# Kernel optimization log

Measured on AMD Instinct MI355X. Metric: run time of the kernel, lower is better.

## Reference

```python
import jax, jax.numpy as jnp
import numpy as np

B, T, E, A, D, S, N, K = 256, 64, 1024, 32, 1024, 256, 1024, 5
MIN_STD = 0.1


def setup_inputs() -> dict:
    key = jax.random.key(0)
    ks = jax.random.split(key, 16)
    def w(k, shape, scale=0.02):
        return jax.random.normal(k, shape, jnp.float32) * scale
    return dict(
        seq_len=T,
        obs_embed=jax.random.normal(ks[0], (B, T, E), jnp.float32),
        action=jax.random.normal(ks[1], (B, T, A), jnp.float32),
        nonterms=jnp.ones((B, T, 1), jnp.float32),
        init_deter=jax.random.normal(ks[2], (B, D), jnp.float32),
        init_stoch=jax.random.normal(ks[3], (B, S), jnp.float32),
        noise_prior=jax.random.normal(ks[4], (T - 1, B, S), jnp.float32),
        noise_post=jax.random.normal(ks[5], (T - 1, B, S), jnp.float32),
        W_embed=w(ks[6], (S + A, D)), b_embed=jnp.zeros((D,), jnp.float32),
        W_ens=w(ks[7], (K, D, S)), b_ens=jnp.zeros((K, S), jnp.float32),
        W_ih=w(ks[8], (3 * D, D)), W_hh=w(ks[9], (3 * D, D)),
        b_ih=jnp.zeros((3 * D,), jnp.float32), b_hh=jnp.zeros((3 * D,), jnp.float32),
        Wp1=w(ks[10], (D, N)), bp1=jnp.zeros((N,), jnp.float32),
        Wp2=w(ks[11], (N, 2 * S)), bp2=jnp.zeros((2 * S,), jnp.float32),
        Wq1=w(ks[12], (D + E, N)), bq1=jnp.zeros((N,), jnp.float32),
        Wq2=w(ks[13], (N, 2 * S)), bq2=jnp.zeros((2 * S,), jnp.float32),
    )


def _rollout(obs_embed, action, nonterms, init_deter, init_stoch,
             noise_prior, noise_post, W_embed, b_embed, W_ens, b_ens,
             W_ih, W_hh, b_ih, b_hh, Wp1, bp1, Wp2, bp2, Wq1, bq1, Wq2, bq2):
    elu = jax.nn.elu

    def gru(x, h):  # torch.nn.GRUCell math
        gi = x @ W_ih.T + b_ih
        gh = h @ W_hh.T + b_hh
        ir, iz, ig = jnp.split(gi, 3, axis=-1)
        hr, hz, hg = jnp.split(gh, 3, axis=-1)
        r = jax.nn.sigmoid(ir + hr)
        z = jax.nn.sigmoid(iz + hz)
        n = jnp.tanh(ig + r * hg)
        return (1.0 - z) * n + z * h

    def step(carry, xs):
        deter, stoch = carry
        obs_t, act_t, nt, eps_p, eps_q = xs  # nt: [B,1]
        prev_action = act_t * nt
        sa = elu(jnp.concatenate([stoch * nt, prev_action], -1) @ W_embed + b_embed)
        preds = jnp.einsum('bd,kds->kbs', sa, W_ens) + b_ens[:, None, :]  # ensemble heads
        deter_new = gru(sa, deter * nt)
        pm, ps = jnp.split(elu(deter_new @ Wp1 + bp1) @ Wp2 + bp2, 2, -1)
        ps = jax.nn.softplus(ps) + MIN_STD
        prior_stoch = pm + ps * eps_p
        qm, qs = jnp.split(elu(jnp.concatenate([deter_new, obs_t], -1) @ Wq1 + bq1) @ Wq2 + bq2, 2, -1)
        qs = jax.nn.softplus(qs) + MIN_STD
        post_stoch = qm + qs * eps_q
        prior_cat = jnp.concatenate([pm, ps, prior_stoch, deter_new], -1)   # [B, 3S+D]
        post_cat = jnp.concatenate([qm, qs, post_stoch, deter_new], -1)     # [B, 3S+D]
        disag_flat = jnp.transpose(preds, (1, 0, 2)).reshape(preds.shape[1], -1)  # [B, K*S]
        out = jnp.concatenate([prior_cat, post_cat, disag_flat], -1)
        return (deter_new, post_stoch), out

    Tm1 = noise_prior.shape[0]
    xs = (jnp.swapaxes(obs_embed[:, :Tm1], 0, 1),
          jnp.swapaxes(action[:, :Tm1], 0, 1),
          jnp.swapaxes(nonterms[:, :Tm1], 0, 1),
          noise_prior, noise_post)
    _, outs = jax.lax.scan(step, (init_deter, init_stoch), xs)
    return jnp.swapaxes(outs, 0, 1)  # [B, T-1, 2*(3S+D)+K*S]


def reference(seq_len, obs_embed, action, nonterms, init_deter, init_stoch,
              noise_prior, noise_post, W_embed, b_embed, W_ens, b_ens,
              W_ih, W_hh, b_ih, b_hh, Wp1, bp1, Wp2, bp2, Wq1, bq1, Wq2, bq2):
    return _rollout(obs_embed, action, nonterms, init_deter, init_stoch,
                    noise_prior, noise_post, W_embed, b_embed, W_ens, b_ens,
                    W_ih, W_hh, b_ih, b_hh, Wp1, bp1, Wp2, bp2, Wq1, bq1, Wq2, bq2)
```

## Files before the change

kernel.cpp:

```cpp
#include <hip/hip_runtime.h>

typedef float f32x4 __attribute__((ext_vector_type(4)));
typedef __bf16 bf16x8 __attribute__((ext_vector_type(8)));
typedef unsigned short u16;

#define NB 256
#define TT 64
#define TM1 63
#define DD 1024
#define SS 256
#define EE 1024
#define AD 32
#define OUTC 4864
#define OUTT ((size_t)TM1 * OUTC)

__device__ __forceinline__ u16 f2bf(float f) {
    unsigned u = __float_as_uint(f);
    u += 0x7FFFu + ((u >> 16) & 1u);
    return (u16)(u >> 16);
}
__device__ __forceinline__ float sigm(float x) { return 1.f / (1.f + expf(-x)); }
__device__ __forceinline__ float splus(float x) { return x > 15.f ? x : log1pf(expf(x)); }
__device__ __forceinline__ float eluf(float x) { return x > 0.f ? x : (expf(x) - 1.f); }
__device__ __forceinline__ int swz(int row, int cb) { return row * 128 + (cb ^ ((row & 7) << 4)); }

template <class FA, class FE>
__device__ __forceinline__ void gemm_tile(char* As, char* Bs, FA fa,
                                          const u16* __restrict__ Bt, int ldb,
                                          int K, int m0, int n0, FE fe) {
    const int tid = threadIdx.x;
    const int lane = tid & 63;
    const int w = tid >> 6;
    const int wr = (w >> 1) * 32, wc = (w & 1) * 32;
    f32x4 acc00 = {}, acc01 = {}, acc10 = {}, acc11 = {};
    const int r0 = tid >> 3;
    const int ke = (tid & 7) * 8;
    const int cb = (tid & 7) * 16;

    for (int k0 = 0; k0 < K; k0 += 64) {
        uint4 av0 = fa(m0 + r0, k0 + ke);
        uint4 av1 = fa(m0 + r0 + 32, k0 + ke);
        uint4 bv0 = *(const uint4*)(Bt + (size_t)(n0 + r0) * ldb + k0 + ke);
        uint4 bv1 = *(const uint4*)(Bt + (size_t)(n0 + r0 + 32) * ldb + k0 + ke);
        __syncthreads();
        *(uint4*)(As + swz(r0, cb)) = av0;
        *(uint4*)(As + swz(r0 + 32, cb)) = av1;
        *(uint4*)(Bs + swz(r0, cb)) = bv0;
        *(uint4*)(Bs + swz(r0 + 32, cb)) = bv1;
        __syncthreads();
#pragma unroll
        for (int kk = 0; kk < 64; kk += 32) {
            const int fcb = kk * 2 + (lane >> 4) * 16;
            bf16x8 a0 = *(const bf16x8*)(As + swz(wr + (lane & 15), fcb));
            bf16x8 a1 = *(const bf16x8*)(As + swz(wr + 16 + (lane & 15), fcb));
            bf16x8 b0 = *(const bf16x8*)(Bs + swz(wc + (lane & 15), fcb));
            bf16x8 b1 = *(const bf16x8*)(Bs + swz(wc + 16 + (lane & 15), fcb));
            acc00 = __builtin_amdgcn_mfma_f32_16x16x32_bf16(a0, b0, acc00, 0, 0, 0);
            acc01 = __builtin_amdgcn_mfma_f32_16x16x32_bf16(a0, b1, acc01, 0, 0, 0);
            acc10 = __builtin_amdgcn_mfma_f32_16x16x32_bf16(a1, b0, acc10, 0, 0, 0);
            acc11 = __builtin_amdgcn_mfma_f32_16x16x32_bf16(a1, b1, acc11, 0, 0, 0);
        }
    }
    const int er = (lane >> 4) * 4, ec = lane & 15;
#pragma unroll
    for (int r = 0; r < 4; r++) {
        fe(m0 + wr + er + r, n0 + wc + ec, acc00[r]);
        fe(m0 + wr + er + r, n0 + wc + 16 + ec, acc01[r]);
        fe(m0 + wr + 16 + er + r, n0 + wc + ec, acc10[r]);
        fe(m0 + wr + 16 + er + r, n0 + wc + 16 + ec, acc11[r]);
    }
}

__global__ void __launch_bounds__(256) k_cast(const float* __restrict__ in,
                                              u16* __restrict__ out, int n) {
    int i = blockIdx.x * 256 + threadIdx.x;
    if (i < n) out[i] = f2bf(in[i]);
}

__global__ void __launch_bounds__(256) k_transpose(const float* __restrict__ in,
                                                   u16* __restrict__ out,
                                                   int R, int C, int Rpad, int total) {
    int i = blockIdx.x * 256 + threadIdx.x;
    if (i >= total) return;
    int r = i % Rpad;
    int bc = i / Rpad;
    int c = bc % C;
    int bb = bc / C;
    out[i] = (r < R) ? f2bf(in[((size_t)bb * R + r) * C + c]) : (u16)0;
}

__global__ void __launch_bounds__(256) k_prep0(const float* __restrict__ init_deter,
                                               const float* __restrict__ init_stoch,
                                               const float* __restrict__ action,
                                               const float* __restrict__ nonterms,
                                               float* __restrict__ deter,
                                               u16* __restrict__ h_nt,
                                               u16* __restrict__ x_embed) {
    int idx = blockIdx.x * 256 + threadIdx.x;
    int b = idx >> 10, d = idx & 1023;
    float nt0 = nonterms[b * TT + 0];
    float dv = init_deter[idx];
    deter[idx] = dv;
    h_nt[idx] = f2bf(dv * nt0);
    if (d < 256) {
        x_embed[b * 320 + d] = f2bf(init_stoch[b * 256 + d] * nt0);
    } else if (d < 320) {
        int c = d - 256;
        x_embed[b * 320 + d] = (c < AD) ? f2bf(action[(size_t)b * TT * AD + c] * nt0) : (u16)0;
    }
}

__global__ void __launch_bounds__(256) k_gru(const float* __restrict__ gi,
                                             const float* __restrict__ gh,
                                             float* __restrict__ deter,
                                             const float* __restrict__ nonterms, int t,
                                             u16* __restrict__ deter_b,
                                             float* __restrict__ out) {
    int idx = blockIdx.x * 256 + threadIdx.x;
    int b = idx >> 10, d = idx & 1023;
    float nt = nonterms[b * TT + t];
    float h = deter[idx] * nt;
    size_t gb = (size_t)b * 3072;
    float r = sigm(gi[gb + d] + gh[gb + d]);
    float z = sigm(gi[gb + 1024 + d] + gh[gb + 1024 + d]);
    float n = tanhf(gi[gb + 2048 + d] + r * gh[gb + 2048 + d]);
    float dn = (1.f - z) * n + z * h;
    deter[idx] = dn;
    deter_b[idx] = f2bf(dn);
    float* ob = out + (size_t)b * OUTT + (size_t)t * OUTC;
    ob[768 + d] = dn;
    ob[2560 + d] = dn;
}

__global__ void __launch_bounds__(256) k_dist(const float* __restrict__ pout,
                                              const float* __restrict__ qout,
                                              const float* __restrict__ noise_p,
                                              const float* __restrict__ noise_q, int t,
                                              const float* __restrict__ deter,
                                              const float* __restrict__ action,
                                              const float* __restrict__ nonterms,
                                              float* __restrict__ out,
                                              u16* __restrict__ x_embed,
                                              u16* __restrict__ h_nt) {
    int idx = blockIdx.x * 256 + threadIdx.x;
    int b = idx >> 10, d = idx & 1023;
    float ntn = nonterms[b * TT + (t + 1)];
    h_nt[idx] = f2bf(deter[idx] * ntn);
    float* ob = out + (size_t)b * OUTT + (size_t)t * OUTC;
    if (d < 256) {
        int s = d;
        float pm = pout[b * 512 + s];
        float ps = splus(pout[b * 512 + 256 + s]) + 0.1f;
        float ep = noise_p[(size_t)t * (NB * SS) + b * SS + s];
        float pst = pm + ps * ep;
        ob[s] = pm;
        ob[256 + s] = ps;
        ob[512 + s] = pst;
        float qm = qout[b * 512 + s];
        float qs = splus(qout[b * 512 + 256 + s]) + 0.1f;
        float eq = noise_q[(size_t)t * (NB * SS) + b * SS + s];
        float qst = qm + qs * eq;
        ob[1792 + s] = qm;
        ob[2048 + s] = qs;
        ob[2304 + s] = qst;
        x_embed[b * 320 + s] = f2bf(qst * ntn);
    } else if (d < 320) {
        int c = d - 256;
        u16 v = 0;
        if (c < AD) v = f2bf(action[(size_t)b * TT * AD + (size_t)(t + 1) * AD + c] * ntn);
        x_embed[b * 320 + 256 + c] = v;
    }
}

__global__ void __launch_bounds__(256) k_gemm_sa(const u16* __restrict__ xe,
                                                 const u16* __restrict__ Wt,
                                                 const float* __restrict__ bias,
                                                 u16* __restrict__ sa) {
    __shared__ char As[8192];
    __shared__ char Bs[8192];
    int m0 = blockIdx.y * 64, n0 = blockIdx.x * 64;
    auto fa = [&](int r, int k) { return *(const uint4*)(xe + r * 320 + k); };
    auto fe = [&](int r, int n, float v) {
        v = eluf(v + bias[n]);
        sa[r * 1024 + n] = f2bf(v);
    };
    gemm_tile(As, Bs, fa, Wt, 320, 320, m0, n0, fe);
}

__global__ void __launch_bounds__(256) k_gemm_big(const u16* __restrict__ sa,
                                                  const u16* __restrict__ hnt,
                                                  const u16* __restrict__ Wih,
                                                  const u16* __restrict__ Whh,
                                                  const u16* __restrict__ Wens,
                                                  const float* __restrict__ bih,
                                                  const float* __restrict__ bhh,
                                                  const float* __restrict__ bens,
                                                  float* __restrict__ gi,
                                                  float* __restrict__ gh,
                                                  float* __restrict__ dout, int t) {
    __shared__ char As[8192];
    __shared__ char Bs[8192];
    int z = blockIdx.z;
    int m0 = blockIdx.y * 64, n0 = blockIdx.x * 64;
    if (z == 2 && n0 >= 1280) return;
    const u16* Ap = (z == 1) ? hnt : sa;
    auto fa = [&](int r, int k) { return *(const uint4*)(Ap + r * 1024 + k); };
    if (z == 0) {
        auto fe = [&](int r, int n, float v) { gi[(size_t)r * 3072 + n] = v + bih[n]; };
        gemm_tile(As, Bs, fa, Wih, 1024, 1024, m0, n0, fe);
    } else if (z == 1) {
        auto fe = [&](int r, int n, float v) { gh[(size_t)r * 3072 + n] = v + bhh[n]; };
        gemm_tile(As, Bs, fa, Whh, 1024, 1024, m0, n0, fe);
    } else {
        float* op = dout + (size_t)t * OUTC + 3584;
        auto fe = [&](int r, int n, float v) { op[(size_t)r * OUTT + n] = v + bens[n]; };
        gemm_tile(As, Bs, fa, Wens, 1024, 1024, m0, n0, fe);
    }
}

__global__ void __launch_bounds__(256) k_gemm_hpq(const u16* __restrict__ dtb,
                                                  const float* __restrict__ obs,
                                                  const u16* __restrict__ Wp1t,
                                                  const u16* __restrict__ Wq1t,
                                                  const float* __restrict__ bp1,
                                                  const float* __restrict__ bq1,
                                                  u16* __restrict__ hp,
                                                  u16* __restrict__ hq, int t) {
    __shared__ char As[8192];
    __shared__ char Bs[8192];
    int z = blockIdx.z;
    int m0 = blockIdx.y * 64, n0 = blockIdx.x * 64;
    if (z == 0) {
        auto fa = [&](int r, int k) { return *(const uint4*)(dtb + r * 1024 + k); };
        auto fe = [&](int r, int n, float v) {
            v = eluf(v + bp1[n]);
            hp[r * 1024 + n] = f2bf(v);
        };
        gemm_tile(As, Bs, fa, Wp1t, 1024, 1024, m0, n0, fe);
    } else {
        auto fa = [&](int r, int k) {
            if (k < 1024) return *(const uint4*)(dtb + r * 1024 + k);
            const float* q = obs + (size_t)r * (TT * EE) + (size_t)t * EE + (k - 1024);
            float4 f0 = *(const float4*)q, f1 = *(const float4*)(q + 4);
            union { u16 u[8]; uint4 v; } x;
            x.u[0] = f2bf(f0.x); x.u[1] = f2bf(f0.y); x.u[2] = f2bf(f0.z); x.u[3] = f2bf(f0.w);
            x.u[4] = f2bf(f1.x); x.u[5] = f2bf(f1.y); x.u[6] = f2bf(f1.z); x.u[7] = f2bf(f1.w);
            return x.v;
        };
        auto fe = [&](int r, int n, float v) {
            v = eluf(v + bq1[n]);
            hq[r * 1024 + n] = f2bf(v);
        };
        gemm_tile(As, Bs, fa, Wq1t, 2048, 2048, m0, n0, fe);
    }
}

__global__ void __launch_bounds__(256) k_gemm_pq(const u16* __restrict__ hp,
                                                 const u16* __restrict__ hq,
                                                 const u16* __restrict__ Wp2t,
                                                 const u16* __restrict__ Wq2t,
                                                 const float* __restrict__ bp2,
                                                 const float* __restrict__ bq2,
                                                 float* __restrict__ pout,
                                                 float* __restrict__ qout) {
    __shared__ char As[8192];
    __shared__ char Bs[8192];
    int z = blockIdx.z;
    int m0 = blockIdx.y * 64, n0 = blockIdx.x * 64;
    const u16* Ap = z ? hq : hp;
    const u16* Bp = z ? Wq2t : Wp2t;
    const float* bb = z ? bq2 : bp2;
    float* op = z ? qout : pout;
    auto fa = [&](int r, int k) { return *(const uint4*)(Ap + r * 1024 + k); };
    auto fe = [&](int r, int n, float v) { op[r * 512 + n] = v + bb[n]; };
    gemm_tile(As, Bs, fa, Bp, 1024, 1024, m0, n0, fe);
}

extern "C" void kernel_launch(void* const* d_in, const int* in_sizes, int n_in,
                              void* d_out, int out_size, void* d_ws, size_t ws_size,
                              hipStream_t stream) {
    const float* obs = (const float*)d_in[1];
    const float* action = (const float*)d_in[2];
    const float* nonterms = (const float*)d_in[3];
    const float* init_deter = (const float*)d_in[4];
    const float* init_stoch = (const float*)d_in[5];
    const float* noise_p = (const float*)d_in[6];
    const float* noise_q = (const float*)d_in[7];
    const float* W_embed = (const float*)d_in[8];
    const float* b_embed = (const float*)d_in[9];
    const float* W_ens = (const float*)d_in[10];
    const float* b_ens = (const float*)d_in[11];
    const float* W_ih = (const float*)d_in[12];
    const float* W_hh = (const float*)d_in[13];
    const float* b_ih = (const float*)d_in[14];
    const float* b_hh = (const float*)d_in[15];
    const float* Wp1 = (const float*)d_in[16];
    const float* bp1 = (const float*)d_in[17];
    const float* Wp2 = (const float*)d_in[18];
    const float* bp2 = (const float*)d_in[19];
    const float* Wq1 = (const float*)d_in[20];
    const float* bq1 = (const float*)d_in[21];
    const float* Wq2 = (const float*)d_in[22];
    const float* bq2 = (const float*)d_in[23];
    float* out = (float*)d_out;

    char* ws = (char*)d_ws;
    size_t off = 0;
    auto alloc = [&](size_t bytes) {
        void* p = ws + off;
        off += (bytes + 255) & ~(size_t)255;
        return p;
    };
    u16* Wembed_t = (u16*)alloc(1024 * 320 * 2);
    u16* Wih_b = (u16*)alloc(3072 * 1024 * 2);
    u16* Whh_b = (u16*)alloc(3072 * 1024 * 2);
    u16* Wens_t = (u16*)alloc(1280 * 1024 * 2);
    u16* Wp1_t = (u16*)alloc(1024 * 1024 * 2);
    u16* Wp2_t = (u16*)alloc(512 * 1024 * 2);
    u16* Wq1_t = (u16*)alloc((size_t)1024 * 2048 * 2);
    u16* Wq2_t = (u16*)alloc(512 * 1024 * 2);
    u16* x_embed = (u16*)alloc(256 * 320 * 2);
    u16* h_nt = (u16*)alloc(256 * 1024 * 2);
    u16* sa = (u16*)alloc(256 * 1024 * 2);
    float* deter = (float*)alloc(256 * 1024 * 4);
    u16* deter_b = (u16*)alloc(256 * 1024 * 2);
    float* gi = (float*)alloc((size_t)256 * 3072 * 4);
    float* gh = (float*)alloc((size_t)256 * 3072 * 4);
    u16* hp = (u16*)alloc(256 * 1024 * 2);
    u16* hq = (u16*)alloc(256 * 1024 * 2);
    float* pout = (float*)alloc(256 * 512 * 4);
    float* qout = (float*)alloc(256 * 512 * 4);
    (void)ws_size;

    {
        int tot = 1024 * 320;
        k_transpose<<<(tot + 255) / 256, 256, 0, stream>>>(W_embed, Wembed_t, 288, 1024, 320, tot);
        int nc = 3072 * 1024;
        k_cast<<<(nc + 255) / 256, 256, 0, stream>>>(W_ih, Wih_b, nc);
        k_cast<<<(nc + 255) / 256, 256, 0, stream>>>(W_hh, Whh_b, nc);
        tot = 5 * 256 * 1024;
        k_transpose<<<(tot + 255) / 256, 256, 0, stream>>>(W_ens, Wens_t, 1024, 256, 1024, tot);
        tot = 1024 * 1024;
        k_transpose<<<(tot + 255) / 256, 256, 0, stream>>>(Wp1, Wp1_t, 1024, 1024, 1024, tot);
        tot = 512 * 1024;
        k_transpose<<<(tot + 255) / 256, 256, 0, stream>>>(Wp2, Wp2_t, 1024, 512, 1024, tot);
        tot = 1024 * 2048;
        k_transpose<<<(tot + 255) / 256, 256, 0, stream>>>(Wq1, Wq1_t, 2048, 1024, 2048, tot);
        tot = 512 * 1024;
        k_transpose<<<(tot + 255) / 256, 256, 0, stream>>>(Wq2, Wq2_t, 1024, 512, 1024, tot);
    }

    k_prep0<<<1024, 256, 0, stream>>>(init_deter, init_stoch, action, nonterms,
                                      deter, h_nt, x_embed);

    for (int t = 0; t < TM1; t++) {
        k_gemm_sa<<<dim3(16, 4), 256, 0, stream>>>(x_embed, Wembed_t, b_embed, sa);
        k_gemm_big<<<dim3(48, 4, 3), 256, 0, stream>>>(sa, h_nt, Wih_b, Whh_b, Wens_t,
                                                       b_ih, b_hh, b_ens, gi, gh, out, t);
        k_gru<<<1024, 256, 0, stream>>>(gi, gh, deter, nonterms, t, deter_b, out);
        k_gemm_hpq<<<dim3(16, 4, 2), 256, 0, stream>>>(deter_b, obs, Wp1_t, Wq1_t,
                                                       bp1, bq1, hp, hq, t);
        k_gemm_pq<<<dim3(8, 4, 2), 256, 0, stream>>>(hp, hq, Wp2_t, Wq2_t, bp2, bq2,
                                                     pout, qout);
        k_dist<<<1024, 256, 0, stream>>>(pout, qout, noise_p, noise_q, t, deter,
                                         action, nonterms, out, x_embed, h_nt);
    }
}
```

Baseline: 4.888 ms.

## Hoist non-recurrent GEMMs out of the time loop and batch them across steps

Restructures the rollout so only the recurrent path stays inside the per-step loop. The observation part of the posterior MLP is computed for all steps up front, and the ensemble heads and prior MLP are run in large batched GEMMs after the loop from stored sa and deter histories. The change also register-prefetches the next K-slice in the GEMM tile, computes several N tiles per block, fuses the softplus/sampling into GEMM epilogues, and switches to fast exp/log/tanh. This removes kernel launches and small-GEMM underutilization per step, at the cost of large history buffers and slightly lower transcendental accuracy.

```diff
diff --git a/kernel.cpp b/kernel.cpp
--- a/kernel.cpp
+++ b/kernel.cpp
@@ -4,70 +4,97 @@
 typedef __bf16 bf16x8 __attribute__((ext_vector_type(8)));
 typedef unsigned short u16;
 
-#define NB 256
-#define TT 64
-#define TM1 63
-#define DD 1024
-#define SS 256
-#define EE 1024
-#define AD 32
 #define OUTC 4864
-#define OUTT ((size_t)TM1 * OUTC)
+#define OUTT ((size_t)63 * OUTC)
 
 __device__ __forceinline__ u16 f2bf(float f) {
     unsigned u = __float_as_uint(f);
     u += 0x7FFFu + ((u >> 16) & 1u);
     return (u16)(u >> 16);
 }
-__device__ __forceinline__ float sigm(float x) { return 1.f / (1.f + expf(-x)); }
-__device__ __forceinline__ float splus(float x) { return x > 15.f ? x : log1pf(expf(x)); }
-__device__ __forceinline__ float eluf(float x) { return x > 0.f ? x : (expf(x) - 1.f); }
+__device__ __forceinline__ float bf2f(u16 h) { return __uint_as_float((unsigned)h << 16); }
+__device__ __forceinline__ float fexp(float x) { return __expf(x); }
+__device__ __forceinline__ float eluf(float x) { return x > 0.f ? x : fexp(x) - 1.f; }
+__device__ __forceinline__ float splus(float x) { return x > 15.f ? x : __logf(1.f + fexp(x)); }
+__device__ __forceinline__ float sigm(float x) { return 1.f / (1.f + fexp(-x)); }
+__device__ __forceinline__ float tanhfast(float x) { return 2.f / (1.f + fexp(-2.f * x)) - 1.f; }
 __device__ __forceinline__ int swz(int row, int cb) { return row * 128 + (cb ^ ((row & 7) << 4)); }
 
-template <class FA, class FE>
-__device__ __forceinline__ void gemm_tile(char* As, char* Bs, FA fa,
-                                          const u16* __restrict__ Bt, int ldb,
-                                          int K, int m0, int n0, FE fe) {
+template <int NT, class FA, class FE>
+__device__ __forceinline__ void gemmN(char* As, FA fa, const u16* __restrict__ Bt,
+                                      int ldb, int n0, int nstr, int K, int m0, FE fe) {
+    char* Bs = As + 8192;
     const int tid = threadIdx.x;
     const int lane = tid & 63;
     const int w = tid >> 6;
     const int wr = (w >> 1) * 32, wc = (w & 1) * 32;
-    f32x4 acc00 = {}, acc01 = {}, acc10 = {}, acc11 = {};
+    f32x4 acc[NT][4];
+    f32x4 zf = {0.f, 0.f, 0.f, 0.f};
+#pragma unroll
+    for (int j = 0; j < NT; j++)
+#pragma unroll
+        for (int q = 0; q < 4; q++) acc[j][q] = zf;
     const int r0 = tid >> 3;
     const int ke = (tid & 7) * 8;
     const int cb = (tid & 7) * 16;
-
+    uint4 av0 = fa(m0 + r0, ke);
+    uint4 av1 = fa(m0 + r0 + 32, ke);
+    uint4 bv[NT][2];
+#pragma unroll
+    for (int j = 0; j < NT; j++) {
+        bv[j][0] = *(const uint4*)(Bt + (size_t)(n0 + j * nstr + r0) * ldb + ke);
+        bv[j][1] = *(const uint4*)(Bt + (size_t)(n0 + j * nstr + r0 + 32) * ldb + ke);
+    }
     for (int k0 = 0; k0 < K; k0 += 64) {
-        uint4 av0 = fa(m0 + r0, k0 + ke);
-        uint4 av1 = fa(m0 + r0 + 32, k0 + ke);
-        uint4 bv0 = *(const uint4*)(Bt + (size_t)(n0 + r0) * ldb + k0 + ke);
-        uint4 bv1 = *(const uint4*)(Bt + (size_t)(n0 + r0 + 32) * ldb + k0 + ke);
         __syncthreads();
         *(uint4*)(As + swz(r0, cb)) = av0;
         *(uint4*)(As + swz(r0 + 32, cb)) = av1;
-        *(uint4*)(Bs + swz(r0, cb)) = bv0;
-        *(uint4*)(Bs + swz(r0 + 32, cb)) = bv1;
+#pragma unroll
+        for (int j = 0; j < NT; j++) {
+            char* B = Bs + j * 8192;
+            *(uint4*)(B + swz(r0, cb)) = bv[j][0];
+            *(uint4*)(B + swz(r0 + 32, cb)) = bv[j][1];
+        }
         __syncthreads();
+        if (k0 + 64 < K) {
+            int k1 = k0 + 64 + ke;
+            av0 = fa(m0 + r0, k1);
+            av1 = fa(m0 + r0 + 32, k1);
+#pragma unroll
+            for (int j = 0; j < NT; j++) {
+                bv[j][0] = *(const uint4*)(Bt + (size_t)(n0 + j * nstr + r0) * ldb + k1);
+                bv[j][1] = *(const uint4*)(Bt + (size_t)(n0 + j * nstr + r0 + 32) * ldb + k1);
+            }
+        }
 #pragma unroll
         for (int kk = 0; kk < 64; kk += 32) {
             const int fcb = kk * 2 + (lane >> 4) * 16;
             bf16x8 a0 = *(const bf16x8*)(As + swz(wr + (lane & 15), fcb));
             bf16x8 a1 = *(const bf16x8*)(As + swz(wr + 16 + (lane & 15), fcb));
-            bf16x8 b0 = *(const bf16x8*)(Bs + swz(wc + (lane & 15), fcb));
-            bf16x8 b1 = *(const bf16x8*)(Bs + swz(wc + 16 + (lane & 15), fcb));
-            acc00 = __builtin_amdgcn_mfma_f32_16x16x32_bf16(a0, b0, acc00, 0, 0, 0);
-            acc01 = __builtin_amdgcn_mfma_f32_16x16x32_bf16(a0, b1, acc01, 0, 0, 0);
-            acc10 = __builtin_amdgcn_mfma_f32_16x16x32_bf16(a1, b0, acc10, 0, 0, 0);
-            acc11 = __builtin_amdgcn_mfma_f32_16x16x32_bf16(a1, b1, acc11, 0, 0, 0);
+#pragma unroll
+            for (int j = 0; j < NT; j++) {
+                char* B = Bs + j * 8192;
+                bf16x8 b0 = *(const bf16x8*)(B + swz(wc + (lane & 15), fcb));
+                bf16x8 b1 = *(const bf16x8*)(B + swz(wc + 16 + (lane & 15), fcb));
+                acc[j][0] = __builtin_amdgcn_mfma_f32_16x16x32_bf16(a0, b0, acc[j][0], 0, 0, 0);
+                acc[j][1] = __builtin_amdgcn_mfma_f32_16x16x32_bf16(a0, b1, acc[j][1], 0, 0, 0);
+                acc[j][2] = __builtin_amdgcn_mfma_f32_16x16x32_bf16(a1, b0, acc[j][2], 0, 0, 0);
+                acc[j][3] = __builtin_amdgcn_mfma_f32_16x16x32_bf16(a1, b1, acc[j][3], 0, 0, 0);
+            }
         }
     }
     const int er = (lane >> 4) * 4, ec = lane & 15;
 #pragma unroll
-    for (int r = 0; r < 4; r++) {
-        fe(m0 + wr + er + r, n0 + wc + ec, acc00[r]);
-        fe(m0 + wr + er + r, n0 + wc + 16 + ec, acc01[r]);
-        fe(m0 + wr + 16 + er + r, n0 + wc + ec, acc10[r]);
-        fe(m0 + wr + 16 + er + r, n0 + wc + 16 + ec, acc11[r]);
+    for (int q = 0; q < 4; q++) {
+        int rr = m0 + wr + (q >> 1) * 16 + er;
+        int cc = n0 + wc + (q & 1) * 16 + ec;
+#pragma unroll
+        for (int r = 0; r < 4; r++) {
+            float vals[NT];
+#pragma unroll
+            for (int j = 0; j < NT; j++) vals[j] = acc[j][q][r];
+            fe(rr + r, cc, vals);
+        }
     }
 }
 
@@ -89,16 +116,16 @@
     out[i] = (r < R) ? f2bf(in[((size_t)bb * R + r) * C + c]) : (u16)0;
 }
 
-__global__ void __launch_bounds__(256) k_prep0(const float* __restrict__ init_deter,
-                                               const float* __restrict__ init_stoch,
-                                               const float* __restrict__ action,
-                                               const float* __restrict__ nonterms,
-                                               float* __restrict__ deter,
-                                               u16* __restrict__ h_nt,
-                                               u16* __restrict__ x_embed) {
+__global__ void __launch_bounds__(256) k_init(const float* __restrict__ init_deter,
+                                              const float* __restrict__ init_stoch,
+                                              const float* __restrict__ action,
+                                              const float* __restrict__ nonterms,
+                                              float* __restrict__ deter,
+                                              u16* __restrict__ h_nt,
+                                              u16* __restrict__ x_embed) {
     int idx = blockIdx.x * 256 + threadIdx.x;
     int b = idx >> 10, d = idx & 1023;
-    float nt0 = nonterms[b * TT + 0];
+    float nt0 = nonterms[b * 64];
     float dv = init_deter[idx];
     deter[idx] = dv;
     h_nt[idx] = f2bf(dv * nt0);
@@ -106,174 +133,205 @@
         x_embed[b * 320 + d] = f2bf(init_stoch[b * 256 + d] * nt0);
     } else if (d < 320) {
         int c = d - 256;
-        x_embed[b * 320 + d] = (c < AD) ? f2bf(action[(size_t)b * TT * AD + c] * nt0) : (u16)0;
-    }
+        x_embed[b * 320 + d] = (c < 32) ? f2bf(action[(size_t)b * 2048 + c] * nt0) : (u16)0;
+    }
+}
+
+__global__ void __launch_bounds__(256) k_obsc(const float* __restrict__ obs,
+                                              const u16* __restrict__ Wq1o_t,
+                                              u16* __restrict__ OBSC) {
+    __shared__ char sm[40960];
+    int jid = blockIdx.x;
+    int rb = jid >> 2, cg = jid & 3;
+    int m0 = rb * 64, n0 = cg * 256;
+    auto fa = [&](int r, int k) {
+        int tt = r >> 8, bb = r & 255;
+        const float* p = obs + ((size_t)bb * 64 + tt) * 1024 + k;
+        float4 f0 = *(const float4*)p, f1 = *(const float4*)(p + 4);
+        union { u16 h[8]; uint4 q; } x;
+        x.h[0] = f2bf(f0.x); x.h[1] = f2bf(f0.y); x.h[2] = f2bf(f0.z); x.h[3] = f2bf(f0.w);
+        x.h[4] = f2bf(f1.x); x.h[5] = f2bf(f1.y); x.h[6] = f2bf(f1.z); x.h[7] = f2bf(f1.w);
+        return x.q;
+    };
+    auto fe = [&](int r, int n, const float* v) {
+#pragma unroll
+        for (int j = 0; j < 4; j++) OBSC[(size_t)r * 1024 + n + j * 64] = f2bf(v[j]);
+    };
+    gemmN<4>(sm, fa, Wq1o_t, 1024, n0, 64, 1024, m0, fe);
+}
+
+__global__ void __launch_bounds__(256) k_sa(const u16* __restrict__ xe,
+                                            const u16* __restrict__ Wt,
+                                            const float* __restrict__ bias,
+                                            u16* __restrict__ sa) {
+    __shared__ char sm[16384];
+    int m0 = blockIdx.y * 64, n0 = blockIdx.x * 64;
+    auto fa = [&](int r, int k) { return *(const uint4*)(xe + r * 320 + k); };
+    auto fe = [&](int r, int n, const float* v) {
+        sa[r * 1024 + n] = f2bf(eluf(v[0] + bias[n]));
+    };
+    gemmN<1>(sm, fa, Wt, 320, n0, 0, 320, m0, fe);
+}
+
+__global__ void __launch_bounds__(256) k_gemm3072(const u16* __restrict__ A,
+                                                  const u16* __restrict__ B,
+                                                  const float* __restrict__ bias,
+                                                  float* __restrict__ dst) {
+    __shared__ char sm[16384];
+    int m0 = blockIdx.y * 64, n0 = blockIdx.x * 64;
+    auto fa = [&](int r, int k) { return *(const uint4*)(A + r * 1024 + k); };
+    auto fe = [&](int r, int n, const float* v) { dst[(size_t)r * 3072 + n] = v[0] + bias[n]; };
+    gemmN<1>(sm, fa, B, 1024, n0, 0, 1024, m0, fe);
 }
 
 __global__ void __launch_bounds__(256) k_gru(const float* __restrict__ gi,
                                              const float* __restrict__ gh,
                                              float* __restrict__ deter,
                                              const float* __restrict__ nonterms, int t,
-                                             u16* __restrict__ deter_b,
+                                             u16* __restrict__ deter_hist,
+                                             u16* __restrict__ h_nt,
                                              float* __restrict__ out) {
     int idx = blockIdx.x * 256 + threadIdx.x;
     int b = idx >> 10, d = idx & 1023;
-    float nt = nonterms[b * TT + t];
+    float nt = nonterms[b * 64 + t];
     float h = deter[idx] * nt;
     size_t gb = (size_t)b * 3072;
     float r = sigm(gi[gb + d] + gh[gb + d]);
     float z = sigm(gi[gb + 1024 + d] + gh[gb + 1024 + d]);
-    float n = tanhf(gi[gb + 2048 + d] + r * gh[gb + 2048 + d]);
+    float n = tanhfast(gi[gb + 2048 + d] + r * gh[gb + 2048 + d]);
     float dn = (1.f - z) * n + z * h;
     deter[idx] = dn;
-    deter_b[idx] = f2bf(dn);
+    u16 db = f2bf(dn);
+    deter_hist[(size_t)t * 262144 + idx] = db;
+    h_nt[idx] = f2bf(dn * nonterms[b * 64 + t + 1]);
     float* ob = out + (size_t)b * OUTT + (size_t)t * OUTC;
     ob[768 + d] = dn;
     ob[2560 + d] = dn;
 }
 
-__global__ void __launch_bounds__(256) k_dist(const float* __restrict__ pout,
-                                              const float* __restrict__ qout,
-                                              const float* __restrict__ noise_p,
-                                              const float* __restrict__ noise_q, int t,
-                                              const float* __restrict__ deter,
-                                              const float* __restrict__ action,
-                                              const float* __restrict__ nonterms,
-                                              float* __restrict__ out,
-                                              u16* __restrict__ x_embed,
-                                              u16* __restrict__ h_nt) {
-    int idx = blockIdx.x * 256 + threadIdx.x;
-    int b = idx >> 10, d = idx & 1023;
-    float ntn = nonterms[b * TT + (t + 1)];
-    h_nt[idx] = f2bf(deter[idx] * ntn);
-    float* ob = out + (size_t)b * OUTT + (size_t)t * OUTC;
-    if (d < 256) {
-        int s = d;
-        float pm = pout[b * 512 + s];
-        float ps = splus(pout[b * 512 + 256 + s]) + 0.1f;
-        float ep = noise_p[(size_t)t * (NB * SS) + b * SS + s];
-        float pst = pm + ps * ep;
-        ob[s] = pm;
-        ob[256 + s] = ps;
-        ob[512 + s] = pst;
-        float qm = qout[b * 512 + s];
-        float qs = splus(qout[b * 512 + 256 + s]) + 0.1f;
-        float eq = noise_q[(size_t)t * (NB * SS) + b * SS + s];
-        float qst = qm + qs * eq;
-        ob[1792 + s] = qm;
-        ob[2048 + s] = qs;
-        ob[2304 + s] = qst;
-        x_embed[b * 320 + s] = f2bf(qst * ntn);
-    } else if (d < 320) {
-        int c = d - 256;
-        u16 v = 0;
-        if (c < AD) v = f2bf(action[(size_t)b * TT * AD + (size_t)(t + 1) * AD + c] * ntn);
-        x_embed[b * 320 + 256 + c] = v;
-    }
-}
-
-__global__ void __launch_bounds__(256) k_gemm_sa(const u16* __restrict__ xe,
-                                                 const u16* __restrict__ Wt,
-                                                 const float* __restrict__ bias,
-                                                 u16* __restrict__ sa) {
-    __shared__ char As[8192];
-    __shared__ char Bs[8192];
+__global__ void __launch_bounds__(256) k_step4(const u16* __restrict__ h_nt,
+                                               const u16* __restrict__ Whh_b,
+                                               const float* __restrict__ b_hh,
+                                               float* __restrict__ gh,
+                                               const u16* __restrict__ deter_hist,
+                                               const u16* __restrict__ Wq1d_t,
+                                               const float* __restrict__ bq1,
+                                               const u16* __restrict__ OBSC,
+                                               u16* __restrict__ HQ, int t) {
+    __shared__ char sm[16384];
+    int bid = blockIdx.x;
+    if (bid < 192) {
+        if (t >= 62) return;
+        int m0 = (bid / 48) * 64, n0 = (bid % 48) * 64;
+        auto fa = [&](int r, int k) { return *(const uint4*)(h_nt + r * 1024 + k); };
+        auto fe = [&](int r, int n, const float* v) { gh[(size_t)r * 3072 + n] = v[0] + b_hh[n]; };
+        gemmN<1>(sm, fa, Whh_b, 1024, n0, 0, 1024, m0, fe);
+    } else {
+        int j = bid - 192;
+        int m0 = (j / 16) * 64, n0 = (j % 16) * 64;
+        const u16* A = deter_hist + (size_t)t * 262144;
+        const u16* ob = OBSC + (size_t)t * 262144;
+        auto fa = [&](int r, int k) { return *(const uint4*)(A + r * 1024 + k); };
+        auto fe = [&](int r, int n, const float* v) {
+            HQ[r * 1024 + n] = f2bf(eluf(v[0] + bq1[n] + bf2f(ob[r * 1024 + n])));
+        };
+        gemmN<1>(sm, fa, Wq1d_t, 1024, n0, 0, 1024, m0, fe);
+    }
+}
+
+__global__ void __launch_bounds__(256) k_q2dist(const u16* __restrict__ HQ,
+                                                const u16* __restrict__ Wq2_t,
+                                                const float* __restrict__ bq2,
+                                                const float* __restrict__ noise_q,
+                                                const float* __restrict__ nonterms,
+                                                const float* __restrict__ action,
+                                                float* __restrict__ out,
+                                                u16* __restrict__ x_embed, int t) {
+    __shared__ char sm[24576];
+    int bid = blockIdx.x;
+    if (bid < 16) {
+        int m0 = (bid >> 2) * 64, n0 = (bid & 3) * 64;
+        auto fa = [&](int r, int k) { return *(const uint4*)(HQ + r * 1024 + k); };
+        auto fe = [&](int r, int s, const float* v) {
+            float m = v[0] + bq2[s];
+            float sd = splus(v[1] + bq2[s + 256]) + 0.1f;
+            float eps = noise_q[(size_t)t * 65536 + r * 256 + s];
+            float st = m + sd * eps;
+            float* obp = out + (size_t)r * OUTT + (size_t)t * OUTC + 1792;
+            obp[s] = m;
+            obp[256 + s] = sd;
+            obp[512 + s] = st;
+            float ntn = nonterms[r * 64 + t + 1];
+            x_embed[r * 320 + s] = f2bf(st * ntn);
+        };
+        gemmN<2>(sm, fa, Wq2_t, 1024, n0, 256, 1024, m0, fe);
+    } else {
+        for (int i = (bid - 16) * 256 + threadIdx.x; i < 16384; i += 1024) {
+            int b = i >> 6, c = i & 63;
+            float ntn = nonterms[b * 64 + t + 1];
+            u16 v = 0;
+            if (c < 32) v = f2bf(action[(size_t)b * 2048 + (size_t)(t + 1) * 32 + c] * ntn);
+            x_embed[b * 320 + 256 + c] = v;
+        }
+    }
+}
+
+__global__ void __launch_bounds__(256) k_ens(const u16* __restrict__ sa_hist,
+                                             const u16* __restrict__ Wens_t,
+                                             const float* __restrict__ b_ens,
+                                             float* __restrict__ out) {
+    __shared__ char sm[40960];
+    int m0 = blockIdx.y * 64, n0 = blockIdx.x * 256;
+    auto fa = [&](int r, int k) { return *(const uint4*)(sa_hist + (size_t)r * 1024 + k); };
+    auto fe = [&](int r, int cc, const float* v) {
+        int tt = r >> 8, b = r & 255;
+        float* op = out + (size_t)b * OUTT + (size_t)tt * OUTC + 3584;
+#pragma unroll
+        for (int j = 0; j < 4; j++) {
+            int n = cc + j * 64;
+            op[n] = v[j] + b_ens[n];
+        }
+    };
+    gemmN<4>(sm, fa, Wens_t, 1024, n0, 64, 1024, m0, fe);
+}
+
+__global__ void __launch_bounds__(256) k_hp(const u16* __restrict__ deter_hist,
+                                            const u16* __restrict__ Wp1_t,
+                                            const float* __restrict__ bp1,
+                                            u16* __restrict__ HP) {
+    __shared__ char sm[40960];
+    int m0 = blockIdx.y * 64, n0 = blockIdx.x * 256;
+    auto fa = [&](int r, int k) { return *(const uint4*)(deter_hist + (size_t)r * 1024 + k); };
+    auto fe = [&](int r, int cc, const float* v) {
+#pragma unroll
+        for (int j = 0; j < 4; j++) {
+            int n = cc + j * 64;
+            HP[(size_t)r * 1024 + n] = f2bf(eluf(v[j] + bp1[n]));
+        }
+    };
+    gemmN<4>(sm, fa, Wp1_t, 1024, n0, 64, 1024, m0, fe);
+}
+
+__global__ void __launch_bounds__(256) k_p2(const u16* __restrict__ HP,
+                                            const u16* __restrict__ Wp2_t,
+                                            const float* __restrict__ bp2,
+                                            const float* __restrict__ noise_p,
+                                            float* __restrict__ out) {
+    __shared__ char sm[24576];
     int m0 = blockIdx.y * 64, n0 = blockIdx.x * 64;
-    auto fa = [&](int r, int k) { return *(const uint4*)(xe + r * 320 + k); };
-    auto fe = [&](int r, int n, float v) {
-        v = eluf(v + bias[n]);
-        sa[r * 1024 + n] = f2bf(v);
-    };
-    gemm_tile(As, Bs, fa, Wt, 320, 320, m0, n0, fe);
-}
-
-__global__ void __launch_bounds__(256) k_gemm_big(const u16* __restrict__ sa,
-                                                  const u16* __restrict__ hnt,
-                                                  const u16* __restrict__ Wih,
-                                                  const u16* __restrict__ Whh,
-                                                  const u16* __restrict__ Wens,
-                                                  const float* __restrict__ bih,
-                                                  const float* __restrict__ bhh,
-                                                  const float* __restrict__ bens,
-                                                  float* __restrict__ gi,
-                                                  float* __restrict__ gh,
-                                                  float* __restrict__ dout, int t) {
-    __shared__ char As[8192];
-    __shared__ char Bs[8192];
-    int z = blockIdx.z;
-    int m0 = blockIdx.y * 64, n0 = blockIdx.x * 64;
-    if (z == 2 && n0 >= 1280) return;
-    const u16* Ap = (z == 1) ? hnt : sa;
-    auto fa = [&](int r, int k) { return *(const uint4*)(Ap + r * 1024 + k); };
-    if (z == 0) {
-        auto fe = [&](int r, int n, float v) { gi[(size_t)r * 3072 + n] = v + bih[n]; };
-        gemm_tile(As, Bs, fa, Wih, 1024, 1024, m0, n0, fe);
-    } else if (z == 1) {
-        auto fe = [&](int r, int n, float v) { gh[(size_t)r * 3072 + n] = v + bhh[n]; };
-        gemm_tile(As, Bs, fa, Whh, 1024, 1024, m0, n0, fe);
-    } else {
-        float* op = dout + (size_t)t * OUTC + 3584;
-        auto fe = [&](int r, int n, float v) { op[(size_t)r * OUTT + n] = v + bens[n]; };
-        gemm_tile(As, Bs, fa, Wens, 1024, 1024, m0, n0, fe);
-    }
-}
-
-__global__ void __launch_bounds__(256) k_gemm_hpq(const u16* __restrict__ dtb,
-                                                  const float* __restrict__ obs,
-                                                  const u16* __restrict__ Wp1t,
-                                                  const u16* __restrict__ Wq1t,
-                                                  const float* __restrict__ bp1,
-                                                  const float* __restrict__ bq1,
-                                                  u16* __restrict__ hp,
-                                                  u16* __restrict__ hq, int t) {
-    __shared__ char As[8192];
-    __shared__ char Bs[8192];
-    int z = blockIdx.z;
-    int m0 = blockIdx.y * 64, n0 = blockIdx.x * 64;
-    if (z == 0) {
-        auto fa = [&](int r, int k) { return *(const uint4*)(dtb + r * 1024 + k); };
-        auto fe = [&](int r, int n, float v) {
-            v = eluf(v + bp1[n]);
-            hp[r * 1024 + n] = f2bf(v);
-        };
-        gemm_tile(As, Bs, fa, Wp1t, 1024, 1024, m0, n0, fe);
-    } else {
-        auto fa = [&](int r, int k) {
-            if (k < 1024) return *(const uint4*)(dtb + r * 1024 + k);
-            const float* q = obs + (size_t)r * (TT * EE) + (size_t)t * EE + (k - 1024);
-            float4 f0 = *(const float4*)q, f1 = *(const float4*)(q + 4);
-            union { u16 u[8]; uint4 v; } x;
-            x.u[0] = f2bf(f0.x); x.u[1] = f2bf(f0.y); x.u[2] = f2bf(f0.z); x.u[3] = f2bf(f0.w);
-            x.u[4] = f2bf(f1.x); x.u[5] = f2bf(f1.y); x.u[6] = f2bf(f1.z); x.u[7] = f2bf(f1.w);
-            return x.v;
-        };
-        auto fe = [&](int r, int n, float v) {
-            v = eluf(v + bq1[n]);
-            hq[r * 1024 + n] = f2bf(v);
-        };
-        gemm_tile(As, Bs, fa, Wq1t, 2048, 2048, m0, n0, fe);
-    }
-}
-
-__global__ void __launch_bounds__(256) k_gemm_pq(const u16* __restrict__ hp,
-                                                 const u16* __restrict__ hq,
-                                                 const u16* __restrict__ Wp2t,
-                                                 const u16* __restrict__ Wq2t,
-                                                 const float* __restrict__ bp2,
-                                                 const float* __restrict__ bq2,
-                                                 float* __restrict__ pout,
-                                                 float* __restrict__ qout) {
-    __shared__ char As[8192];
-    __shared__ char Bs[8192];
-    int z = blockIdx.z;
-    int m0 = blockIdx.y * 64, n0 = blockIdx.x * 64;
-    const u16* Ap = z ? hq : hp;
-    const u16* Bp = z ? Wq2t : Wp2t;
-    const float* bb = z ? bq2 : bp2;
-    float* op = z ? qout : pout;
-    auto fa = [&](int r, int k) { return *(const uint4*)(Ap + r * 1024 + k); };
-    auto fe = [&](int r, int n, float v) { op[r * 512 + n] = v + bb[n]; };
-    gemm_tile(As, Bs, fa, Bp, 1024, 1024, m0, n0, fe);
+    auto fa = [&](int r, int k) { return *(const uint4*)(HP + (size_t)r * 1024 + k); };
+    auto fe = [&](int r, int s, const float* v) {
+        int tt = r >> 8, b = r & 255;
+        float m = v[0] + bp2[s];
+        float sd = splus(v[1] + bp2[s + 256]) + 0.1f;
+        float eps = noise_p[(size_t)tt * 65536 + b * 256 + s];
+        float st = m + sd * eps;
+        float* obp = out + (size_t)b * OUTT + (size_t)tt * OUTC;
+        obp[s] = m;
+        obp[256 + s] = sd;
+        obp[512 + s] = st;
+    };
+    gemmN<2>(sm, fa, Wp2_t, 1024, n0, 256, 1024, m0, fe);
 }
 
 extern "C" void kernel_launch(void* const* d_in, const int* in_sizes, int n_in,
@@ -311,26 +369,25 @@
         off += (bytes + 255) & ~(size_t)255;
         return p;
     };
-    u16* Wembed_t = (u16*)alloc(1024 * 320 * 2);
-    u16* Wih_b = (u16*)alloc(3072 * 1024 * 2);
-    u16* Whh_b = (u16*)alloc(3072 * 1024 * 2);
-    u16* Wens_t = (u16*)alloc(1280 * 1024 * 2);
-    u16* Wp1_t = (u16*)alloc(1024 * 1024 * 2);
-    u16* Wp2_t = (u16*)alloc(512 * 1024 * 2);
-    u16* Wq1_t = (u16*)alloc((size_t)1024 * 2048 * 2);
-    u16* Wq2_t = (u16*)alloc(512 * 1024 * 2);
-    u16* x_embed = (u16*)alloc(256 * 320 * 2);
-    u16* h_nt = (u16*)alloc(256 * 1024 * 2);
-    u16* sa = (u16*)alloc(256 * 1024 * 2);
-    float* deter = (float*)alloc(256 * 1024 * 4);
-    u16* deter_b = (u16*)alloc(256 * 1024 * 2);
+    u16* Wembed_t = (u16*)alloc((size_t)1024 * 320 * 2);
+    u16* Wih_b = (u16*)alloc((size_t)3072 * 1024 * 2);
+    u16* Whh_b = (u16*)alloc((size_t)3072 * 1024 * 2);
+    u16* Wens_t = (u16*)alloc((size_t)1280 * 1024 * 2);
+    u16* Wp1_t = (u16*)alloc((size_t)1024 * 1024 * 2);
+    u16* Wp2_t = (u16*)alloc((size_t)512 * 1024 * 2);
+    u16* Wq1d_t = (u16*)alloc((size_t)1024 * 1024 * 2);
+    u16* Wq1o_t = (u16*)alloc((size_t)1024 * 1024 * 2);
+    u16* Wq2_t = (u16*)alloc((size_t)512 * 1024 * 2);
+    u16* OBSC = (u16*)alloc((size_t)16128 * 1024 * 2);
+    u16* sa_hist = (u16*)alloc((size_t)16128 * 1024 * 2);
+    u16* deter_hist = (u16*)alloc((size_t)16128 * 1024 * 2);
+    u16* x_embed = (u16*)alloc((size_t)256 * 320 * 2);
+    u16* h_nt = (u16*)alloc((size_t)256 * 1024 * 2);
+    u16* HQ = (u16*)alloc((size_t)256 * 1024 * 2);
+    float* deter = (float*)alloc((size_t)256 * 1024 * 4);
     float* gi = (float*)alloc((size_t)256 * 3072 * 4);
     float* gh = (float*)alloc((size_t)256 * 3072 * 4);
-    u16* hp = (u16*)alloc(256 * 1024 * 2);
-    u16* hq = (u16*)alloc(256 * 1024 * 2);
-    float* pout = (float*)alloc(256 * 512 * 4);
-    float* qout = (float*)alloc(256 * 512 * 4);
-    (void)ws_size;
+    (void)ws_size; (void)in_sizes; (void)n_in; (void)out_size;
 
     {
         int tot = 1024 * 320;
@@ -344,25 +401,30 @@
         k_transpose<<<(tot + 255) / 256, 256, 0, stream>>>(Wp1, Wp1_t, 1024, 1024, 1024, tot);
         tot = 512 * 1024;
         k_transpose<<<(tot + 255) / 256, 256, 0, stream>>>(Wp2, Wp2_t, 1024, 512, 1024, tot);
-        tot = 1024 * 2048;
-        k_transpose<<<(tot + 255) / 256, 256, 0, stream>>>(Wq1, Wq1_t, 2048, 1024, 2048, tot);
+        tot = 1024 * 1024;
+        k_transpose<<<(tot + 255) / 256, 256, 0, stream>>>(Wq1, Wq1d_t, 1024, 1024, 1024, tot);
+        k_transpose<<<(tot + 255) / 256, 256, 0, stream>>>(Wq1 + 1024 * 1024, Wq1o_t, 1024, 1024, 1024, tot);
         tot = 512 * 1024;
         k_transpose<<<(tot + 255) / 256, 256, 0, stream>>>(Wq2, Wq2_t, 1024, 512, 1024, tot);
     }
-
-    k_prep0<<<1024, 256, 0, stream>>>(init_deter, init_stoch, action, nonterms,
-                                      deter, h_nt, x_embed);
-
-    for (int t = 0; t < TM1; t++) {
-        k_gemm_sa<<<dim3(16, 4), 256, 0, stream>>>(x_embed, Wembed_t, b_embed, sa);
-        k_gemm_big<<<dim3(48, 4, 3), 256, 0, stream>>>(sa, h_nt, Wih_b, Whh_b, Wens_t,
-                                                       b_ih, b_hh, b_ens, gi, gh, out, t);
-        k_gru<<<1024, 256, 0, stream>>>(gi, gh, deter, nonterms, t, deter_b, out);
-        k_gemm_hpq<<<dim3(16, 4, 2), 256, 0, stream>>>(deter_b, obs, Wp1_t, Wq1_t,
-                                                       bp1, bq1, hp, hq, t);
-        k_gemm_pq<<<dim3(8, 4, 2), 256, 0, stream>>>(hp, hq, Wp2_t, Wq2_t, bp2, bq2,
-                                                     pout, qout);
-        k_dist<<<1024, 256, 0, stream>>>(pout, qout, noise_p, noise_q, t, deter,
-                                         action, nonterms, out, x_embed, h_nt);
-    }
-}
+    k_init<<<1024, 256, 0, stream>>>(init_deter, init_stoch, action, nonterms,
+                                     deter, h_nt, x_embed);
+    k_obsc<<<1008, 256, 0, stream>>>(obs, Wq1o_t, OBSC);
+    k_gemm3072<<<dim3(48, 4), 256, 0, stream>>>(h_nt, Whh_b, b_hh, gh);
+
+    for (int t = 0; t < 63; t++) {
+        u16* sa_t = sa_hist + (size_t)t * 262144;
+        k_sa<<<dim3(16, 4), 256, 0, stream>>>(x_embed, Wembed_t, b_embed, sa_t);
+        k_gemm3072<<<dim3(48, 4), 256, 0, stream>>>(sa_t, Wih_b, b_ih, gi);
+        k_gru<<<1024, 256, 0, stream>>>(gi, gh, deter, nonterms, t, deter_hist, h_nt, out);
+        k_step4<<<256, 256, 0, stream>>>(h_nt, Whh_b, b_hh, gh, deter_hist, Wq1d_t,
+                                         bq1, OBSC, HQ, t);
+        k_q2dist<<<20, 256, 0, stream>>>(HQ, Wq2_t, bq2, noise_q, nonterms, action,
+                                         out, x_embed, t);
+    }
+
+    k_ens<<<dim3(5, 252), 256, 0, stream>>>(sa_hist, Wens_t, b_ens, out);
+    u16* HP = OBSC;
+    k_hp<<<dim3(4, 252), 256, 0, stream>>>(deter_hist, Wp1_t, bp1, HP);
+    k_p2<<<dim3(4, 252), 256, 0, stream>>>(HP, Wp2_t, bp2, noise_p, out);
+}
```

Result: slower. 5.471 ms (+11.9%).
